# Kernel tuning notes

Hardware: AMD Instinct MI355X
Metric: run time of the kernel (lower is better)

Reference implementation:

```python
import jax, jax.numpy as jnp
import numpy as np

NEG = jnp.float32(-1e30)  # finite stand-in for -inf (keeps vjp NaN-free)


def setup_inputs() -> dict:
    key = jax.random.key(0)
    k1, k2, k3 = jax.random.split(key, 3)
    B, T, C, L = 64, 128, 6625, 25
    predicts = jax.random.normal(k1, (B, T, C), dtype=jnp.float32)
    # blank=0, so valid label ids are 1..C-1
    labels = jax.random.randint(k2, (B, L), 1, C).astype(jnp.int64)
    label_lengths = jax.random.randint(k3, (B,), 1, L + 1).astype(jnp.int64)
    return {"predicts": predicts, "labels": labels, "label_lengths": label_lengths}


def _ctc_loss(log_probs, labels, label_lengths, blank=0):
    # log_probs: [T, B, C]; labels: [B, L]; label_lengths: [B]
    T, B, C = log_probs.shape
    L = labels.shape[1]
    S = 2 * L + 1
    # extended label sequence with interleaved blanks: [B, S]
    ext = jnp.full((B, S), blank, dtype=jnp.int32)
    ext = ext.at[:, 1::2].set(labels.astype(jnp.int32))
    # transition from s-2 allowed iff ext[s] != blank and ext[s] != ext[s-2]
    ext_sm2 = jnp.pad(ext[:, :-2], ((0, 0), (2, 0)), constant_values=blank)
    skip_ok = (ext != blank) & (ext != ext_sm2)  # [B, S]

    def lp_ext(lp_t):  # [B, C] -> [B, S], gather per-symbol log-probs
        return jnp.take_along_axis(lp_t, ext, axis=1)

    # alpha init at t=0
    lp0 = lp_ext(log_probs[0])
    alpha0 = jnp.full((B, S), NEG)
    alpha0 = alpha0.at[:, 0].set(lp0[:, 0])
    alpha0 = alpha0.at[:, 1].set(lp0[:, 1])

    def step(alpha, lp_t):
        a1 = jnp.pad(alpha[:, :-1], ((0, 0), (1, 0)), constant_values=NEG)
        a2 = jnp.pad(alpha[:, :-2], ((0, 0), (2, 0)), constant_values=NEG)
        a2 = jnp.where(skip_ok, a2, NEG)
        m = jnp.maximum(jnp.maximum(alpha, a1), a2)
        lse = m + jnp.log(jnp.exp(alpha - m) + jnp.exp(a1 - m) + jnp.exp(a2 - m))
        return lse + lp_ext(lp_t), None

    alphaT, _ = jax.lax.scan(step, alpha0, log_probs[1:])  # [B, S]

    # total log-likelihood ends at s = 2*len (blank) or s = 2*len - 1 (last label)
    idx_last = (2 * label_lengths).astype(jnp.int32)
    aL = jnp.take_along_axis(alphaT, idx_last[:, None], axis=1)[:, 0]
    aP = jnp.take_along_axis(alphaT, (idx_last - 1)[:, None], axis=1)[:, 0]
    m = jnp.maximum(aL, aP)
    loss = -(m + jnp.log(jnp.exp(aL - m) + jnp.exp(aP - m)))
    # zero_infinity=True
    loss = jnp.where(loss < 1e29, loss, 0.0)
    return loss  # [B]


def reference(predicts, labels, label_lengths):
    # predicts: [B, T, C] -> [T, B, C], then log_softmax over classes
    log_probs = jax.nn.log_softmax(jnp.transpose(predicts, (1, 0, 2)), axis=2)
    loss = _ctc_loss(log_probs, labels, label_lengths, blank=0)
    return jnp.mean(loss)
```

## Files before the change

### kernel.cpp

```cpp
#include <hip/hip_runtime.h>
#include <stdint.h>
#include <math.h>

constexpr int B = 64, T = 128, C = 6625, L = 25;
constexpr int S = 2 * L + 1;
constexpr int NCLS = L + 1;

#define LOG2E  1.44269504088896340736f
#define LN2    0.69314718055994530942f
#define NEG2   (-1.4426950408889634e30f)
#define NEGINF (-1e38f)

__device__ inline float dpp_shup1(float x, float fill) {
    const int r = __builtin_amdgcn_update_dpp(
        __float_as_int(fill), __float_as_int(x), 0x138, 0xF, 0xF, false);
    return __int_as_float(r);
}

template <bool GATHER>
__global__ __launch_bounds__(256) void k_lse_gather(
    const float* __restrict__ predicts, const int* __restrict__ labels,
    float* __restrict__ lse_out, float* __restrict__ lp_out,
    float* __restrict__ out)
{
    const int row = blockIdx.x;
    const int b   = row >> 7;
    const int tid = threadIdx.x;
    const float* rp = predicts + (size_t)row * C;

    if (row == 0 && tid == 255) out[0] = 0.0f;

    const int mis  = (int)(((uintptr_t)rp >> 2) & 3);
    const int head = (4 - mis) & 3;
    const int nvec = (C - head) >> 2;
    const int tail = C - head - (nvec << 2);
    const float4* vp = (const float4*)(rp + head);

    float4 v[7];
#pragma unroll
    for (int j = 0; j < 7; ++j) {
        const int i = tid + j * 256;
        v[j] = (i < nvec) ? vp[i] : make_float4(NEGINF, NEGINF, NEGINF, NEGINF);
    }
    float sc = NEGINF;
    if (tid < head)                      sc = rp[tid];
    else if (tid >= 4 && tid < 4 + tail) sc = rp[head + (nvec << 2) + (tid - 4)];

    float s0 = __expf(sc), s1 = 0.0f, s2 = 0.0f, s3 = 0.0f;
#pragma unroll
    for (int j = 0; j < 7; ++j) {
        s0 += __expf(v[j].x); s1 += __expf(v[j].y);
        s2 += __expf(v[j].z); s3 += __expf(v[j].w);
    }
    float s = (s0 + s1) + (s2 + s3);

    const int wave = tid >> 6, lane = tid & 63;
    for (int off = 32; off; off >>= 1) s += __shfl_down(s, off);
    __shared__ float ssum[4];
    if (lane == 0) ssum[wave] = s;
    __syncthreads();
    const float lse = __logf((ssum[0] + ssum[1]) + (ssum[2] + ssum[3]));

    if (GATHER) {
        if (tid < NCLS) {
            const int cls = (tid == 0) ? 0 : labels[b * L + tid - 1];
            lp_out[(size_t)row * NCLS + tid] = (rp[cls] - lse) * LOG2E;
        }
    } else {
        if (tid == 0) lse_out[row] = lse;
    }
}

template <bool USE_LP>
__global__ __launch_bounds__(64) void k_ctc(
    const float* __restrict__ predicts, const int* __restrict__ labels,
    const int* __restrict__ lens, const float* __restrict__ lse,
    const float* __restrict__ lp_ws, float* __restrict__ out)
{
    const int b = blockIdx.x;
    const int s = threadIdx.x;
    const int  li = s >> 1;
    const bool isLab = (s & 1) && (s < S);

    const int myLab = isLab ? labels[b * L + li] : 0;
    const bool allow_skip = isLab && (s >= 3) && (myLab != labels[b * L + li - 1]);
    const int  k   = isLab ? (1 + li) : 0;
    const int  cls = isLab ? myLab : 0;

    auto fetch = [&](int t) -> float {
        const int row = b * T + t;
        if (USE_LP) return lp_ws[(size_t)row * NCLS + k];
        else        return (predicts[(size_t)row * C + cls] - lse[row]) * LOG2E;
    };
    auto step = [&](float& alpha, float lp2) {
        const float a1 = dpp_shup1(alpha, NEG2);
        float       a2 = dpp_shup1(a1,    NEG2);
        if (!allow_skip) a2 = NEG2;
        const float mm  = fmaxf(alpha, fmaxf(a1, a2));
        const float sum = exp2f(alpha - mm) + exp2f(a1 - mm) + exp2f(a2 - mm);
        alpha = mm + log2f(sum) + lp2;
    };

    constexpr int CH = 16;
    float Av[CH], Bv[CH];
#pragma unroll
    for (int i = 0; i < CH; ++i) Av[i] = fetch(i);
    float alpha = (s <= 1) ? Av[0] : NEG2;

#pragma unroll
    for (int t0 = 0; t0 < T; t0 += 2 * CH) {
#pragma unroll
        for (int i = 0; i < CH; ++i) { const int tt = t0 + CH + i;     Bv[i] = (tt < T) ? fetch(tt) : 0.0f; }
#pragma unroll
        for (int i = 0; i < CH; ++i) { if (t0 == 0 && i == 0) continue; step(alpha, Av[i]); }
#pragma unroll
        for (int i = 0; i < CH; ++i) { const int tt = t0 + 2 * CH + i; Av[i] = (tt < T) ? fetch(tt) : 0.0f; }
#pragma unroll
        for (int i = 0; i < CH; ++i) step(alpha, Bv[i]);
    }

    const int len = lens[b];
    const int idx = 2 * len;
    const float aL = __shfl(alpha, idx);
    const float aP = __shfl(alpha, idx - 1);
    if (s == 0) {
        const float mm = fmaxf(aL, aP);
        float loss = -(mm + log2f(exp2f(aL - mm) + exp2f(aP - mm))) * LN2;
        if (!(loss < 1e29f)) loss = 0.0f;
        atomicAdd(out, loss * (1.0f / (float)B));
    }
}

extern "C" void kernel_launch(void* const* d_in, const int* in_sizes, int n_in,
                              void* d_out, int out_size, void* d_ws, size_t ws_size,
                              hipStream_t stream)
{
    const float* predicts = (const float*)d_in[0];
    const int*   labels   = (const int*)d_in[1];
    const int*   lens     = (const int*)d_in[2];
    float*       out      = (float*)d_out;

    char* ws = (char*)d_ws;
    const size_t lp_bytes = (size_t)B * T * NCLS * sizeof(float);

    if (ws_size >= lp_bytes) {
        float* lp_ws = (float*)ws;
        k_lse_gather<true><<<B * T, 256, 0, stream>>>(predicts, labels, nullptr, lp_ws, out);
        k_ctc<true><<<B, 64, 0, stream>>>(predicts, labels, lens, nullptr, lp_ws, out);
    } else {
        float* lse_ws = (float*)ws;
        k_lse_gather<false><<<B * T, 256, 0, stream>>>(predicts, labels, lse_ws, nullptr, out);
        k_ctc<false><<<B, 64, 0, stream>>>(predicts, labels, lens, lse_ws, nullptr, out);
    }
}
```

Measured before the change: 52.72 us.

## Fuse log-sum-exp and CTC recursion into one kernel with atomic handoff

Merges the row log-sum-exp pass and the CTC alpha recursion into a single launch. The first B blocks run the recursion on raw logits scaled to log2 and so overlap with the softmax-normalizer blocks. Because every path at time t collects one lp term, the per-time log-normalizers are subtracted once at the end as a sum, and the recursion blocks spin on per-batch counters to wait for them. A global counter lets the last finishing block do the mean, which replaces the atomicAdd into out. In exchange it adds a memset launch and relies on the spinning recursion blocks being co-resident with the producer blocks.

```diff
diff --git a/kernel.cpp b/kernel.cpp
--- a/kernel.cpp
+++ b/kernel.cpp
@@ -4,7 +4,6 @@
 
 constexpr int B = 64, T = 128, C = 6625, L = 25;
 constexpr int S = 2 * L + 1;
-constexpr int NCLS = L + 1;
 
 #define LOG2E  1.44269504088896340736f
 #define LN2    0.69314718055994530942f
@@ -17,81 +16,70 @@
     return __int_as_float(r);
 }
 
-template <bool GATHER>
-__global__ __launch_bounds__(256) void k_lse_gather(
+__global__ __launch_bounds__(256) void k_fused(
     const float* __restrict__ predicts, const int* __restrict__ labels,
-    float* __restrict__ lse_out, float* __restrict__ lp_out,
-    float* __restrict__ out)
-{
-    const int row = blockIdx.x;
-    const int b   = row >> 7;
+    const int* __restrict__ lens, float* __restrict__ sumexp,
+    float* __restrict__ loss_ws, uint32_t* __restrict__ cnt,
+    uint32_t* __restrict__ gcnt, float* __restrict__ out)
+{
+    const int bid = blockIdx.x;
     const int tid = threadIdx.x;
-    const float* rp = predicts + (size_t)row * C;
-
-    if (row == 0 && tid == 255) out[0] = 0.0f;
-
-    const int mis  = (int)(((uintptr_t)rp >> 2) & 3);
-    const int head = (4 - mis) & 3;
-    const int nvec = (C - head) >> 2;
-    const int tail = C - head - (nvec << 2);
-    const float4* vp = (const float4*)(rp + head);
-
-    float4 v[7];
-#pragma unroll
-    for (int j = 0; j < 7; ++j) {
-        const int i = tid + j * 256;
-        v[j] = (i < nvec) ? vp[i] : make_float4(NEGINF, NEGINF, NEGINF, NEGINF);
-    }
-    float sc = NEGINF;
-    if (tid < head)                      sc = rp[tid];
-    else if (tid >= 4 && tid < 4 + tail) sc = rp[head + (nvec << 2) + (tid - 4)];
-
-    float s0 = __expf(sc), s1 = 0.0f, s2 = 0.0f, s3 = 0.0f;
-#pragma unroll
-    for (int j = 0; j < 7; ++j) {
-        s0 += __expf(v[j].x); s1 += __expf(v[j].y);
-        s2 += __expf(v[j].z); s3 += __expf(v[j].w);
-    }
-    float s = (s0 + s1) + (s2 + s3);
-
-    const int wave = tid >> 6, lane = tid & 63;
-    for (int off = 32; off; off >>= 1) s += __shfl_down(s, off);
-    __shared__ float ssum[4];
-    if (lane == 0) ssum[wave] = s;
-    __syncthreads();
-    const float lse = __logf((ssum[0] + ssum[1]) + (ssum[2] + ssum[3]));
-
-    if (GATHER) {
-        if (tid < NCLS) {
-            const int cls = (tid == 0) ? 0 : labels[b * L + tid - 1];
-            lp_out[(size_t)row * NCLS + tid] = (rp[cls] - lse) * LOG2E;
+
+    if (bid >= B) {
+        const int row = bid - B;
+        const int b   = row >> 7;
+        const float* rp = predicts + (size_t)row * C;
+
+        const int mis  = (int)(((uintptr_t)rp >> 2) & 3);
+        const int head = (4 - mis) & 3;
+        const int nvec = (C - head) >> 2;
+        const int tail = C - head - (nvec << 2);
+        const float4* vp = (const float4*)(rp + head);
+
+        float4 v[7];
+#pragma unroll
+        for (int j = 0; j < 7; ++j) {
+            const int i = tid + j * 256;
+            v[j] = (i < nvec) ? vp[i] : make_float4(NEGINF, NEGINF, NEGINF, NEGINF);
         }
-    } else {
-        if (tid == 0) lse_out[row] = lse;
-    }
-}
-
-template <bool USE_LP>
-__global__ __launch_bounds__(64) void k_ctc(
-    const float* __restrict__ predicts, const int* __restrict__ labels,
-    const int* __restrict__ lens, const float* __restrict__ lse,
-    const float* __restrict__ lp_ws, float* __restrict__ out)
-{
-    const int b = blockIdx.x;
-    const int s = threadIdx.x;
-    const int  li = s >> 1;
+        float sc = NEGINF;
+        if (tid < head)                      sc = rp[tid];
+        else if (tid >= 4 && tid < 4 + tail) sc = rp[head + (nvec << 2) + (tid - 4)];
+
+        float s0 = __expf(sc), s1 = 0.0f, s2 = 0.0f, s3 = 0.0f;
+#pragma unroll
+        for (int j = 0; j < 7; ++j) {
+            s0 += __expf(v[j].x); s1 += __expf(v[j].y);
+            s2 += __expf(v[j].z); s3 += __expf(v[j].w);
+        }
+        float s = (s0 + s1) + (s2 + s3);
+
+        for (int off = 32; off; off >>= 1) s += __shfl_down(s, off);
+        __shared__ float ssum[4];
+        if ((tid & 63) == 0) ssum[tid >> 6] = s;
+        __syncthreads();
+        if (tid == 0) {
+            const float tot = (ssum[0] + ssum[1]) + (ssum[2] + ssum[3]);
+            __hip_atomic_store(&sumexp[row], tot,
+                               __ATOMIC_RELAXED, __HIP_MEMORY_SCOPE_AGENT);
+            asm volatile("s_waitcnt vmcnt(0)" ::: "memory");
+            __hip_atomic_fetch_add(&cnt[b], 1u,
+                                   __ATOMIC_RELAXED, __HIP_MEMORY_SCOPE_AGENT);
+        }
+        return;
+    }
+
+    if (tid >= 64) return;
+    const int b = bid;
+    const int s = tid;
+    const int  li  = (s >> 1) < L ? (s >> 1) : (L - 1);
     const bool isLab = (s & 1) && (s < S);
-
     const int myLab = isLab ? labels[b * L + li] : 0;
     const bool allow_skip = isLab && (s >= 3) && (myLab != labels[b * L + li - 1]);
-    const int  k   = isLab ? (1 + li) : 0;
-    const int  cls = isLab ? myLab : 0;
-
-    auto fetch = [&](int t) -> float {
-        const int row = b * T + t;
-        if (USE_LP) return lp_ws[(size_t)row * NCLS + k];
-        else        return (predicts[(size_t)row * C + cls] - lse[row]) * LOG2E;
-    };
+    const int cls = isLab ? myLab : 0;
+
+    const float* pb = predicts + (size_t)b * T * C + cls;
+    auto fetch = [&](int t) -> float { return pb[(size_t)t * C] * LOG2E; };
     auto step = [&](float& alpha, float lp2) {
         const float a1 = dpp_shup1(alpha, NEG2);
         float       a2 = dpp_shup1(a1,    NEG2);
@@ -119,6 +107,86 @@
         for (int i = 0; i < CH; ++i) step(alpha, Bv[i]);
     }
 
+    while (__hip_atomic_load(&cnt[b], __ATOMIC_RELAXED,
+                             __HIP_MEMORY_SCOPE_AGENT) < (uint32_t)T)
+        __builtin_amdgcn_s_sleep(2);
+
+    const float se0 = __hip_atomic_load(&sumexp[b * T + s],
+                                        __ATOMIC_RELAXED, __HIP_MEMORY_SCOPE_AGENT);
+    const float se1 = __hip_atomic_load(&sumexp[b * T + 64 + s],
+                                        __ATOMIC_RELAXED, __HIP_MEMORY_SCOPE_AGENT);
+    float l2 = log2f(se0) + log2f(se1);
+    for (int off = 32; off; off >>= 1) l2 += __shfl_down(l2, off);
+
+    const int len = lens[b];
+    const int idx = 2 * len;
+    const float aL = __shfl(alpha, idx);
+    const float aP = __shfl(alpha, idx - 1);
+    uint32_t g = 0;
+    if (s == 0) {
+        const float mm   = fmaxf(aL, aP);
+        const float comb = mm + log2f(exp2f(aL - mm) + exp2f(aP - mm));
+        float loss = -(comb - l2) * LN2;
+        if (!(loss < 1e29f)) loss = 0.0f;
+        __hip_atomic_store(&loss_ws[b], loss,
+                           __ATOMIC_RELAXED, __HIP_MEMORY_SCOPE_AGENT);
+        asm volatile("s_waitcnt vmcnt(0)" ::: "memory");
+        g = __hip_atomic_fetch_add(gcnt, 1u,
+                                   __ATOMIC_RELAXED, __HIP_MEMORY_SCOPE_AGENT) + 1u;
+    }
+    g = __shfl(g, 0);
+    if (g != (uint32_t)B) return;
+
+    float vs = __hip_atomic_load(&loss_ws[s],
+                                 __ATOMIC_RELAXED, __HIP_MEMORY_SCOPE_AGENT);
+    for (int off = 32; off; off >>= 1) vs += __shfl_down(vs, off);
+    if (s == 0) out[0] = vs * (1.0f / (float)B);
+}
+
+__global__ __launch_bounds__(256) void k_lse_only(
+    const float* __restrict__ predicts, float* __restrict__ lse_out,
+    float* __restrict__ out)
+{
+    const int row = blockIdx.x;
+    const int tid = threadIdx.x;
+    const float* rp = predicts + (size_t)row * C;
+    if (row == 0 && tid == 255) out[0] = 0.0f;
+
+    float s = 0.0f;
+    for (int c = tid; c < C; c += 256) s += __expf(rp[c]);
+    for (int off = 32; off; off >>= 1) s += __shfl_down(s, off);
+    __shared__ float ssum[4];
+    if ((tid & 63) == 0) ssum[tid >> 6] = s;
+    __syncthreads();
+    if (tid == 0) lse_out[row] = __logf((ssum[0] + ssum[1]) + (ssum[2] + ssum[3]));
+}
+
+__global__ __launch_bounds__(64) void k_ctc_slow(
+    const float* __restrict__ predicts, const int* __restrict__ labels,
+    const int* __restrict__ lens, const float* __restrict__ lse,
+    float* __restrict__ out)
+{
+    const int b = blockIdx.x;
+    const int s = threadIdx.x;
+    const int li = (s >> 1) < L ? (s >> 1) : (L - 1);
+    const bool isLab = (s & 1) && (s < S);
+    const int myLab = isLab ? labels[b * L + li] : 0;
+    const bool allow_skip = isLab && (s >= 3) && (myLab != labels[b * L + li - 1]);
+    const int cls = isLab ? myLab : 0;
+
+    auto fetch = [&](int t) -> float {
+        const int row = b * T + t;
+        return (predicts[(size_t)row * C + cls] - lse[row]) * LOG2E;
+    };
+    float alpha = (s <= 1) ? fetch(0) : NEG2;
+    for (int t = 1; t < T; ++t) {
+        const float lpt = fetch(t);
+        const float a1 = dpp_shup1(alpha, NEG2);
+        float       a2 = dpp_shup1(a1,    NEG2);
+        if (!allow_skip) a2 = NEG2;
+        const float mm  = fmaxf(alpha, fmaxf(a1, a2));
+        alpha = mm + log2f(exp2f(alpha - mm) + exp2f(a1 - mm) + exp2f(a2 - mm)) + lpt;
+    }
     const int len = lens[b];
     const int idx = 2 * len;
     const float aL = __shfl(alpha, idx);
@@ -141,15 +209,23 @@
     float*       out      = (float*)d_out;
 
     char* ws = (char*)d_ws;
-    const size_t lp_bytes = (size_t)B * T * NCLS * sizeof(float);
-
-    if (ws_size >= lp_bytes) {
-        float* lp_ws = (float*)ws;
-        k_lse_gather<true><<<B * T, 256, 0, stream>>>(predicts, labels, nullptr, lp_ws, out);
-        k_ctc<true><<<B, 64, 0, stream>>>(predicts, labels, lens, nullptr, lp_ws, out);
+    const size_t se_bytes  = (size_t)B * T * sizeof(float);
+    const size_t loss_off  = se_bytes;
+    const size_t cnt_off   = loss_off + 256;
+    const size_t gcnt_off  = cnt_off + B * sizeof(uint32_t);
+    const size_t need      = gcnt_off + sizeof(uint32_t);
+
+    if (ws_size >= need) {
+        float*    sumexp  = (float*)ws;
+        float*    loss_ws = (float*)(ws + loss_off);
+        uint32_t* cnt     = (uint32_t*)(ws + cnt_off);
+        uint32_t* gcnt    = (uint32_t*)(ws + gcnt_off);
+        hipMemsetAsync(ws + cnt_off, 0, (B + 1) * sizeof(uint32_t), stream);
+        k_fused<<<B + B * T, 256, 0, stream>>>(predicts, labels, lens,
+                                               sumexp, loss_ws, cnt, gcnt, out);
     } else {
         float* lse_ws = (float*)ws;
-        k_lse_gather<false><<<B * T, 256, 0, stream>>>(predicts, labels, lse_ws, nullptr, out);
-        k_ctc<false><<<B, 64, 0, stream>>>(predicts, labels, lens, lse_ws, nullptr, out);
-    }
-}
+        k_lse_only<<<B * T, 256, 0, stream>>>(predicts, lse_ws, out);
+        k_ctc_slow<<<B, 64, 0, stream>>>(predicts, labels, lens, lse_ws, out);
+    }
+}
```

New measurement: 101.3 us. 1.92x slower.
